# Performance work log

Measured on AMD Instinct MI355X. Metric: run time of the kernel, lower is better.

## Reference

```python
import jax, jax.numpy as jnp
import numpy as np

N, D, E, H, K = 8192, 1024, 8, 256, 2


def setup_inputs() -> dict:
    key = jax.random.key(0)
    ks = jax.random.split(key, 9)
    s = 0.02
    return {
        "x": jax.random.normal(ks[0], (N, D), dtype=jnp.float32),
        "Wg": jax.random.normal(ks[1], (D, E), dtype=jnp.float32) * s,
        "bg": jnp.zeros((E,), dtype=jnp.float32),
        "W1": jax.random.normal(ks[2], (E, D, H), dtype=jnp.float32) * s,
        "b1": jnp.zeros((E, H), dtype=jnp.float32),
        "W2": jax.random.normal(ks[3], (E, H, H), dtype=jnp.float32) * s,
        "b2": jnp.zeros((E, H), dtype=jnp.float32),
        "W3": jax.random.normal(ks[4], (E, H, D), dtype=jnp.float32) * s,
        "b3": jnp.zeros((E, D), dtype=jnp.float32),
    }


def reference(x, Wg, bg, W1, b1, W2, b2, W3, b3):
    # Gating: softmax over experts, then keep only top-k gate values per token.
    gates = jax.nn.softmax(x @ Wg + bg, axis=-1)              # [N, E]
    top_v, top_i = jax.lax.top_k(gates, K)                    # [N, K]
    rows = jnp.arange(gates.shape[0])[:, None]                # [N, 1]
    top_k_gates = jnp.zeros_like(gates).at[rows, top_i].set(top_v)  # [N, E]

    # Dense all-expert MLP (matches original: every expert runs on every token).
    h = jax.nn.relu(jnp.einsum('nd,edh->neh', x, W1) + b1)    # [N, E, H]
    h = jax.nn.relu(jnp.einsum('neh,ehg->neg', h, W2) + b2)   # [N, E, H]  (dropout is eval no-op)
    eo = jax.nn.relu(jnp.einsum('neh,ehd->ned', h, W3) + b3)  # [N, E, D]

    # Combine with masked gates: einsum('...nde,...ne->...nd') with eo in 'ned' layout.
    output = jnp.einsum('ned,ne->nd', eo, top_k_gates)        # [N, D]
    return output
```

## Files before the change

kernel.cpp:

```cpp
#include <hip/hip_runtime.h>
#include <math.h>

#define NTOK 8192
#define DDIM 1024
#define NEXP 8
#define HDIM 256
#define TOPK 2
#define PADM 128
#define CAPS (NTOK * TOPK + NEXP * PADM)
#define NT64  (CAPS / 64)
#define NT128 (CAPS / 128)

typedef __attribute__((ext_vector_type(8))) __bf16 bf16x8;
typedef __attribute__((ext_vector_type(4))) float f32x4;

#define GLDS16(g, s)                                                      \
    __builtin_amdgcn_global_load_lds(                                     \
        (const __attribute__((address_space(1))) void*)(g),               \
        (__attribute__((address_space(3))) void*)(s), 16, 0, 0)

static constexpr size_t OFF_TOFF = 128;
static constexpr size_t OFF_ZBUF = 4096;
static constexpr size_t OFF_T2E  = 8192;
static constexpr size_t OFF_T2G  = OFF_T2E + (size_t)NTOK * TOPK * 4;
static constexpr size_t OFF_SLOT = OFF_T2G + (size_t)NTOK * TOPK * 4;
static constexpr size_t OFF_TOK  = OFF_SLOT + (size_t)NTOK * TOPK * 4;
static constexpr size_t OFF_GAT  = OFF_TOK + (size_t)CAPS * 4;
static constexpr size_t OFF_XB   = (OFF_GAT + (size_t)CAPS * 4 + 255) & ~(size_t)255;
static constexpr size_t OFF_W1T  = OFF_XB  + (size_t)NTOK * DDIM * 2;
static constexpr size_t OFF_W2T  = OFF_W1T + (size_t)NEXP * DDIM * HDIM * 2;
static constexpr size_t OFF_W3T  = OFF_W2T + (size_t)NEXP * HDIM * HDIM * 2;
static constexpr size_t OFF_H2   = OFF_W3T + (size_t)NEXP * HDIM * DDIM * 2;
static constexpr size_t OFF_H3   = OFF_H2  + (size_t)CAPS * HDIM * 2;

static __device__ __forceinline__ unsigned short f2b(float f) {
    __bf16 h = (__bf16)f;
    return __builtin_bit_cast(unsigned short, h);
}
static __device__ __forceinline__ float b2f(unsigned short u) {
    return __builtin_bit_cast(float, ((unsigned)u) << 16);
}

__global__ __launch_bounds__(256) void gate_trans(
    const float* __restrict__ x, const float* __restrict__ Wg,
    const float* __restrict__ bg, unsigned short* __restrict__ xb,
    int* __restrict__ top2e, float* __restrict__ top2g,
    const float* __restrict__ W1, const float* __restrict__ W2,
    const float* __restrict__ W3, __bf16* __restrict__ w1t,
    __bf16* __restrict__ w2t, __bf16* __restrict__ w3t)
{
    __shared__ __align__(16) float sh[NEXP * DDIM];
    const int tid = threadIdx.x;

    if (blockIdx.x < 256) {
        for (int d = tid; d < DDIM; d += 256) {
            const float4 w0 = *(const float4*)(Wg + (size_t)d * NEXP);
            const float4 w1 = *(const float4*)(Wg + (size_t)d * NEXP + 4);
            sh[0 * DDIM + d] = w0.x; sh[1 * DDIM + d] = w0.y;
            sh[2 * DDIM + d] = w0.z; sh[3 * DDIM + d] = w0.w;
            sh[4 * DDIM + d] = w1.x; sh[5 * DDIM + d] = w1.y;
            sh[6 * DDIM + d] = w1.z; sh[7 * DDIM + d] = w1.w;
        }
        __syncthreads();

        const int n = (blockIdx.y * 256 + blockIdx.x) * 4 + (tid >> 6);
        const int lane = tid & 63;
        const float* xr = x + (size_t)n * DDIM;
        unsigned short* xbr = xb + (size_t)n * DDIM;

        float acc[NEXP];
#pragma unroll
        for (int e = 0; e < NEXP; ++e) acc[e] = 0.f;

#pragma unroll
        for (int it = 0; it < 4; ++it) {
            const int d = it * 256 + lane * 4;
            const float4 xv = *(const float4*)(xr + d);
            ushort4 u;
            u.x = f2b(xv.x); u.y = f2b(xv.y); u.z = f2b(xv.z); u.w = f2b(xv.w);
            *(ushort4*)(xbr + d) = u;
#pragma unroll
            for (int e = 0; e < NEXP; ++e) {
                const float4 wt = *(const float4*)(sh + e * DDIM + d);
                acc[e] = fmaf(xv.x, wt.x, acc[e]);
                acc[e] = fmaf(xv.y, wt.y, acc[e]);
                acc[e] = fmaf(xv.z, wt.z, acc[e]);
                acc[e] = fmaf(xv.w, wt.w, acc[e]);
            }
        }
#pragma unroll
        for (int off = 32; off > 0; off >>= 1)
#pragma unroll
            for (int e = 0; e < NEXP; ++e) acc[e] += __shfl_down(acc[e], off, 64);

        if (lane == 0) {
            float v[NEXP], mx = -1e30f;
#pragma unroll
            for (int e = 0; e < NEXP; ++e) { v[e] = acc[e] + bg[e]; mx = fmaxf(mx, v[e]); }
            float p[NEXP], s = 0.f;
#pragma unroll
            for (int e = 0; e < NEXP; ++e) { p[e] = expf(v[e] - mx); s += p[e]; }
            const float inv = 1.f / s;
#pragma unroll
            for (int e = 0; e < NEXP; ++e) p[e] *= inv;
            int i0 = 0;
#pragma unroll
            for (int e = 1; e < NEXP; ++e) if (p[e] > p[i0]) i0 = e;
            int i1 = (i0 == 0) ? 1 : 0;
#pragma unroll
            for (int e = 0; e < NEXP; ++e) if (e != i0 && p[e] > p[i1]) i1 = e;
            top2e[n * 2 + 0] = i0;  top2e[n * 2 + 1] = i1;
            top2g[n * 2 + 0] = p[i0]; top2g[n * 2 + 1] = p[i1];
        }
    } else {
        const int e = blockIdx.y;
        int bt = blockIdx.x - 256;
        const float* Wi; __bf16* Wo; int R, C, xt, yt;
        if (bt < 256)      { Wi = W1; Wo = w1t; R = DDIM; C = HDIM; xt = bt & 7;  yt = bt >> 3; }
        else if (bt < 320) { bt -= 256; Wi = W2; Wo = w2t; R = HDIM; C = HDIM; xt = bt & 7;  yt = bt >> 3; }
        else               { bt -= 320; Wi = W3; Wo = w3t; R = HDIM; C = DDIM; xt = bt & 31; yt = bt >> 5; }
        const int r0 = yt * 32, c0 = xt * 32;
        const int tx = tid & 31, ty = tid >> 5;
        const float* Wie = Wi + (size_t)e * R * C;
        __bf16* Woe = Wo + (size_t)e * C * R;
#pragma unroll
        for (int j = 0; j < 4; ++j)
            sh[(ty + j * 8) * 33 + tx] = Wie[(size_t)(r0 + ty + j * 8) * C + c0 + tx];
        __syncthreads();
#pragma unroll
        for (int j = 0; j < 4; ++j)
            Woe[(size_t)(c0 + ty + j * 8) * R + r0 + tx] = (__bf16)sh[tx * 33 + ty + j * 8];
    }
}

__global__ __launch_bounds__(1024) void route(
    const int* __restrict__ top2e, const float* __restrict__ top2g,
    int* __restrict__ toff, int* __restrict__ tok, float* __restrict__ gat,
    int* __restrict__ slotof, float* __restrict__ zbuf)
{
    const int tid = threadIdx.x;
    const int wv = tid >> 6, ln = tid & 63;
    __shared__ int   waveTot[16][NEXP];
    __shared__ int   waveBase[16][NEXP];
    __shared__ int   totS[NEXP];
    __shared__ int   toffS[NEXP + 1];
    __shared__ short excS[1024][NEXP];

    zbuf[tid] = 0.f;

    int myE[16]; float myG[16];
    const int4*   pe = (const int4*)(top2e + tid * 16);
    const float4* pg = (const float4*)(top2g + tid * 16);
#pragma unroll
    for (int q = 0; q < 4; ++q) {
        const int4 v = pe[q];
        myE[q * 4 + 0] = v.x; myE[q * 4 + 1] = v.y;
        myE[q * 4 + 2] = v.z; myE[q * 4 + 3] = v.w;
        const float4 g = pg[q];
        myG[q * 4 + 0] = g.x; myG[q * 4 + 1] = g.y;
        myG[q * 4 + 2] = g.z; myG[q * 4 + 3] = g.w;
    }

#pragma unroll
    for (int e = 0; e < NEXP; ++e) {
        int c = 0;
#pragma unroll
        for (int j = 0; j < 16; ++j) c += (myE[j] == e);
        int inc = c;
#pragma unroll
        for (int off = 1; off < 64; off <<= 1) {
            const int t = __shfl_up(inc, off, 64);
            if (ln >= off) inc += t;
        }
        excS[tid][e] = (short)(inc - c);
        if (ln == 63) waveTot[wv][e] = inc;
    }
    __syncthreads();

    if (tid < NEXP) {
        int b = 0;
#pragma unroll
        for (int w = 0; w < 16; ++w) {
            const int t = waveTot[w][tid];
            waveBase[w][tid] = b;
            b += t;
        }
        totS[tid] = b;
    }
    __syncthreads();

    if (tid == 0) {
        int acc = 0;
#pragma unroll
        for (int e = 0; e < NEXP; ++e) {
            toffS[e] = acc;
            acc += (totS[e] + PADM - 1) & ~(PADM - 1);
        }
        toffS[NEXP] = acc;
#pragma unroll
        for (int e = 0; e <= NEXP; ++e) toff[e] = toffS[e];
    }
    __syncthreads();

#pragma unroll
    for (int j = 0; j < 16; ++j) {
        int pre = 0;
#pragma unroll
        for (int j2 = 0; j2 < j; ++j2) pre += (myE[j2] == myE[j]);
        const int e = myE[j];
        const int slot = toffS[e] + waveBase[wv][e] + (int)excS[tid][e] + pre;
        const int i = tid * 16 + j;
        tok[slot] = i >> 1;
        gat[slot] = myG[j];
        slotof[i] = slot;
    }

#pragma unroll
    for (int e = 0; e < NEXP; ++e) {
        const int begin = toffS[e] + totS[e];
        const int end   = toffS[e + 1];
        for (int i = begin + tid; i < end; i += 1024) {
            tok[i] = -1;
            gat[i] = 0.f;
        }
    }
}

__global__ __launch_bounds__(256) void egemm12(
    const __bf16* __restrict__ xb, const __bf16* __restrict__ w1t,
    const __bf16* __restrict__ w2t, const float* __restrict__ b1,
    const float* __restrict__ b2, const int* __restrict__ toff,
    const int* __restrict__ tok, const char* __restrict__ zbuf,
    __bf16* __restrict__ h2)
{
    const int total = toff[NEXP];
    const int slot0 = blockIdx.x * 64;
    if (slot0 >= total) return;
    int e = 0;
    while (toff[e + 1] <= slot0) ++e;

    __shared__ __align__(16) char smem[73728];
    char* AsB = smem;
    char* BsB = smem + 8192;
    char* H1s = smem + 40960;

    const int tid  = threadIdx.x;
    const int lane = tid & 63;
    const int wid  = tid >> 6;

    const int srow  = tid >> 3;
    const int sslot = tid & 7;
    const int ks    = sslot ^ (srow & 7);

    const __bf16* We1 = w1t + (size_t)e * HDIM * DDIM;
    const char* ap[2];
#pragma unroll
    for (int i = 0; i < 2; ++i) {
        const int t = tok[slot0 + i * 32 + srow];
        ap[i] = (t >= 0) ? (const char*)(xb + (size_t)t * DDIM + ks * 8) : zbuf;
    }
    const char* bp1[8];
#pragma unroll
    for (int i = 0; i < 8; ++i)
        bp1[i] = (const char*)(We1 + (size_t)(i * 32 + srow) * DDIM + ks * 8);

    const int llo = lane & 15, lhi = lane >> 4;
    const int m7 = llo & 7;
    int abyte[4], bbyte[4];
#pragma unroll
    for (int m = 0; m < 4; ++m) {
        abyte[m] = (m * 16 + llo) * 128;
        bbyte[m] = (wid * 64 + m * 16 + llo) * 128;
    }

    f32x4 acc[4][4];
#pragma unroll
    for (int m = 0; m < 4; ++m)
#pragma unroll
        for (int n = 0; n < 4; ++n) acc[m][n] = (f32x4){0.f, 0.f, 0.f, 0.f};

    for (int k0 = 0; k0 < DDIM; k0 += 64) {
        const size_t kb = (size_t)k0 * 2;
        GLDS16(ap[0] + kb, AsB + tid * 16);
        GLDS16(ap[1] + kb, AsB + 4096 + tid * 16);
#pragma unroll
        for (int i = 0; i < 8; ++i)
            GLDS16(bp1[i] + kb, BsB + i * 4096 + tid * 16);
        __syncthreads();
#pragma unroll
        for (int kk = 0; kk < 2; ++kk) {
            const int sl = ((kk << 2) + lhi) ^ m7;
            bf16x8 af[4], bfr[4];
#pragma unroll
            for (int m = 0; m < 4; ++m) af[m]  = *(const bf16x8*)(AsB + abyte[m] + (sl << 4));
#pragma unroll
            for (int n = 0; n < 4; ++n) bfr[n] = *(const bf16x8*)(BsB + bbyte[n] + (sl << 4));
#pragma unroll
            for (int m = 0; m < 4; ++m)
#pragma unroll
                for (int n = 0; n < 4; ++n)
                    acc[m][n] = __builtin_amdgcn_mfma_f32_16x16x32_bf16(
                        af[m], bfr[n], acc[m][n], 0, 0, 0);
        }
        __syncthreads();
    }

    {
        const float* be1 = b1 + (size_t)e * HDIM;
#pragma unroll
        for (int n = 0; n < 4; ++n) {
            const int col = wid * 64 + n * 16 + llo;
            const float bb = be1[col];
            const int colbyte = (col & 7) * 2;
            const int slice = col >> 3;
#pragma unroll
            for (int m = 0; m < 4; ++m) {
#pragma unroll
                for (int j = 0; j < 4; ++j) {
                    const int r = m * 16 + lhi * 4 + j;
                    const float v = fmaxf(acc[m][n][j] + bb, 0.f);
                    *(__bf16*)(H1s + r * 512 + ((slice ^ (r & 7)) << 4) + colbyte) = (__bf16)v;
                }
                acc[m][n] = (f32x4){0.f, 0.f, 0.f, 0.f};
            }
        }
    }
    __syncthreads();

    const __bf16* We2 = w2t + (size_t)e * HDIM * HDIM;
    const char* bp2[8];
#pragma unroll
    for (int i = 0; i < 8; ++i)
        bp2[i] = (const char*)(We2 + (size_t)(i * 32 + srow) * HDIM + ks * 8);

    for (int k2 = 0; k2 < 4; ++k2) {
        const size_t kb = (size_t)k2 * 128;
#pragma unroll
        for (int i = 0; i < 8; ++i)
            GLDS16(bp2[i] + kb, BsB + i * 4096 + tid * 16);
        __syncthreads();
#pragma unroll
        for (int kk = 0; kk < 2; ++kk) {
            const int slB = ((kk << 2) + lhi) ^ m7;
            const int sA  = k2 * 8 + (kk << 2) + lhi;
            const int slA = sA ^ m7;
            bf16x8 af[4], bfr[4];
#pragma unroll
            for (int m = 0; m < 4; ++m)
                af[m] = *(const bf16x8*)(H1s + (m * 16 + llo) * 512 + (slA << 4));
#pragma unroll
            for (int n = 0; n < 4; ++n)
                bfr[n] = *(const bf16x8*)(BsB + bbyte[n] + (slB << 4));
#pragma unroll
            for (int m = 0; m < 4; ++m)
#pragma unroll
                for (int n = 0; n < 4; ++n)
                    acc[m][n] = __builtin_amdgcn_mfma_f32_16x16x32_bf16(
                        af[m], bfr[n], acc[m][n], 0, 0, 0);
        }
        __syncthreads();
    }

    {
        const float* be2 = b2 + (size_t)e * HDIM;
#pragma unroll
        for (int n = 0; n < 4; ++n) {
            const int col = wid * 64 + n * 16 + llo;
            const float bb = be2[col];
#pragma unroll
            for (int m = 0; m < 4; ++m) {
#pragma unroll
                for (int j = 0; j < 4; ++j) {
                    const int r = slot0 + m * 16 + lhi * 4 + j;
                    h2[(size_t)r * HDIM + col] = (__bf16)fmaxf(acc[m][n][j] + bb, 0.f);
                }
            }
        }
    }
}

template<int KDIM, int NCOL>
__global__ __launch_bounds__(256) void egemm3(
    const __bf16* __restrict__ Ain, const __bf16* __restrict__ Wt,
    const float* __restrict__ ball, const int* __restrict__ toff,
    const float* __restrict__ gat, __bf16* __restrict__ Out)
{
    const int total = toff[NEXP];
    const int slot0 = blockIdx.y * 128;
    if (slot0 >= total) return;
    int e = 0;
    while (toff[e + 1] <= slot0) ++e;
    const int col0 = blockIdx.x * 128;

    __shared__ __align__(16) char smem[32768];
    char* AsB = smem;
    char* BsB = smem + 16384;

    const int tid  = threadIdx.x;
    const int lane = tid & 63;
    const int wid  = tid >> 6;
    const int wr = wid >> 1, wc = wid & 1;

    const int srow  = tid >> 3;
    const int sslot = tid & 7;
    const int ks    = sslot ^ (srow & 7);
    const __bf16* We = Wt + (size_t)e * NCOL * KDIM;
    const char* ap[4];
    const char* bp[4];
#pragma unroll
    for (int i = 0; i < 4; ++i) {
        const int row = i * 32 + srow;
        ap[i] = (const char*)(Ain + (size_t)(slot0 + row) * KDIM + ks * 8);
        bp[i] = (const char*)(We + (size_t)(col0 + row) * KDIM + ks * 8);
    }

    const int llo = lane & 15, lhi = lane >> 4;
    const int m7 = llo & 7;
    int abyte[4], bbyte[4];
#pragma unroll
    for (int m = 0; m < 4; ++m) {
        abyte[m] = (wr * 64 + m * 16 + llo) * 128;
        bbyte[m] = (wc * 64 + m * 16 + llo) * 128;
    }

    f32x4 acc[4][4];
#pragma unroll
    for (int m = 0; m < 4; ++m)
#pragma unroll
        for (int n = 0; n < 4; ++n) acc[m][n] = (f32x4){0.f, 0.f, 0.f, 0.f};

    for (int k0 = 0; k0 < KDIM; k0 += 64) {
        const size_t kb = (size_t)k0 * 2;
#pragma unroll
        for (int i = 0; i < 4; ++i)
            GLDS16(ap[i] + kb, AsB + i * 4096 + wid * 1024);
#pragma unroll
        for (int i = 0; i < 4; ++i)
            GLDS16(bp[i] + kb, BsB + i * 4096 + wid * 1024);
        __syncthreads();
#pragma unroll
        for (int kk = 0; kk < 2; ++kk) {
            const int sl = ((kk << 2) + lhi) ^ m7;
            bf16x8 af[4], bfr[4];
#pragma unroll
            for (int m = 0; m < 4; ++m) af[m]  = *(const bf16x8*)(AsB + abyte[m] + (sl << 4));
#pragma unroll
            for (int n = 0; n < 4; ++n) bfr[n] = *(const bf16x8*)(BsB + bbyte[n] + (sl << 4));
#pragma unroll
            for (int m = 0; m < 4; ++m)
#pragma unroll
                for (int n = 0; n < 4; ++n)
                    acc[m][n] = __builtin_amdgcn_mfma_f32_16x16x32_bf16(
                        af[m], bfr[n], acc[m][n], 0, 0, 0);
        }
        __syncthreads();
    }

    const float* be = ball + (size_t)e * NCOL;
#pragma unroll
    for (int m = 0; m < 4; ++m) {
        const int rbase = slot0 + wr * 64 + m * 16 + lhi * 4;
        float g[4];
#pragma unroll
        for (int j = 0; j < 4; ++j) g[j] = gat[rbase + j];
#pragma unroll
        for (int n = 0; n < 4; ++n) {
            const int col = col0 + wc * 64 + n * 16 + llo;
            const float bb = be[col];
#pragma unroll
            for (int j = 0; j < 4; ++j) {
                const float v = fmaxf(acc[m][n][j] + bb, 0.f) * g[j];
                Out[(size_t)(rbase + j) * NCOL + col] = (__bf16)v;
            }
        }
    }
}

__global__ __launch_bounds__(256) void combine(
    const unsigned short* __restrict__ h3, const int* __restrict__ slotof,
    float* __restrict__ out)
{
    const int n = blockIdx.x;
    const int c = threadIdx.x * 4;
    const int s0 = slotof[n * 2], s1 = slotof[n * 2 + 1];
    const ushort4 a = *(const ushort4*)(h3 + (size_t)s0 * DDIM + c);
    const ushort4 b = *(const ushort4*)(h3 + (size_t)s1 * DDIM + c);
    float4 o;
    o.x = b2f(a.x) + b2f(b.x);
    o.y = b2f(a.y) + b2f(b.y);
    o.z = b2f(a.z) + b2f(b.z);
    o.w = b2f(a.w) + b2f(b.w);
    *(float4*)(out + (size_t)n * DDIM + c) = o;
}

extern "C" void kernel_launch(void* const* d_in, const int* in_sizes, int n_in,
                              void* d_out, int out_size, void* d_ws, size_t ws_size,
                              hipStream_t stream)
{
    const float* x  = (const float*)d_in[0];
    const float* Wg = (const float*)d_in[1];
    const float* bg = (const float*)d_in[2];
    const float* W1 = (const float*)d_in[3];
    const float* b1 = (const float*)d_in[4];
    const float* W2 = (const float*)d_in[5];
    const float* b2 = (const float*)d_in[6];
    const float* W3 = (const float*)d_in[7];
    const float* b3 = (const float*)d_in[8];
    float* out = (float*)d_out;

    char* ws = (char*)d_ws;
    int*   toff   = (int*)(ws + OFF_TOFF);
    char*  zbuf   = ws + OFF_ZBUF;
    int*   top2e  = (int*)(ws + OFF_T2E);
    float* top2g  = (float*)(ws + OFF_T2G);
    int*   slotof = (int*)(ws + OFF_SLOT);
    int*   tok    = (int*)(ws + OFF_TOK);
    float* gat    = (float*)(ws + OFF_GAT);
    unsigned short* xbu = (unsigned short*)(ws + OFF_XB);
    __bf16* xb  = (__bf16*)(ws + OFF_XB);
    __bf16* w1t = (__bf16*)(ws + OFF_W1T);
    __bf16* w2t = (__bf16*)(ws + OFF_W2T);
    __bf16* w3t = (__bf16*)(ws + OFF_W3T);
    __bf16* h2  = (__bf16*)(ws + OFF_H2);
    __bf16* h3  = (__bf16*)(ws + OFF_H3);

    gate_trans<<<dim3(832, NEXP), 256, 0, stream>>>(
        x, Wg, bg, xbu, top2e, top2g, W1, W2, W3, w1t, w2t, w3t);
    route<<<1, 1024, 0, stream>>>(top2e, top2g, toff, tok, gat, slotof, (float*)zbuf);

    egemm12<<<NT64, 256, 0, stream>>>(xb, w1t, w2t, b1, b2, toff, tok, zbuf, h2);
    egemm3<HDIM, DDIM><<<dim3(DDIM / 128, NT128), 256, 0, stream>>>(
        h2, w3t, b3, toff, gat, h3);

    combine<<<NTOK, 256, 0, stream>>>((const unsigned short*)h3, slotof, out);
}
```

Before: 106.8 us.

## Fuse top-k combine into expert GEMM3 epilogue via atomic adds

Removes the separate combine kernel and the bf16 h3 intermediate buffer. The third expert GEMM now scatters its gated output straight into the fp32 output with unsafeAtomicAdd, indexed by token, and skips padded slots. The output is zeroed inside the gate/transpose kernel. This saves one launch plus a write and re-read of the h3 buffer and the slot map, at the cost of scattered fp32 atomics (two per output element) and an extra full zeroing pass over the output.

```diff
diff --git a/kernel.cpp b/kernel.cpp
--- a/kernel.cpp
+++ b/kernel.cpp
@@ -23,22 +23,17 @@
 static constexpr size_t OFF_ZBUF = 4096;
 static constexpr size_t OFF_T2E  = 8192;
 static constexpr size_t OFF_T2G  = OFF_T2E + (size_t)NTOK * TOPK * 4;
-static constexpr size_t OFF_SLOT = OFF_T2G + (size_t)NTOK * TOPK * 4;
-static constexpr size_t OFF_TOK  = OFF_SLOT + (size_t)NTOK * TOPK * 4;
+static constexpr size_t OFF_TOK  = OFF_T2G + (size_t)NTOK * TOPK * 4;
 static constexpr size_t OFF_GAT  = OFF_TOK + (size_t)CAPS * 4;
 static constexpr size_t OFF_XB   = (OFF_GAT + (size_t)CAPS * 4 + 255) & ~(size_t)255;
 static constexpr size_t OFF_W1T  = OFF_XB  + (size_t)NTOK * DDIM * 2;
 static constexpr size_t OFF_W2T  = OFF_W1T + (size_t)NEXP * DDIM * HDIM * 2;
 static constexpr size_t OFF_W3T  = OFF_W2T + (size_t)NEXP * HDIM * HDIM * 2;
 static constexpr size_t OFF_H2   = OFF_W3T + (size_t)NEXP * HDIM * DDIM * 2;
-static constexpr size_t OFF_H3   = OFF_H2  + (size_t)CAPS * HDIM * 2;
 
 static __device__ __forceinline__ unsigned short f2b(float f) {
     __bf16 h = (__bf16)f;
     return __builtin_bit_cast(unsigned short, h);
-}
-static __device__ __forceinline__ float b2f(unsigned short u) {
-    return __builtin_bit_cast(float, ((unsigned)u) << 16);
 }
 
 __global__ __launch_bounds__(256) void gate_trans(
@@ -47,10 +42,18 @@
     int* __restrict__ top2e, float* __restrict__ top2g,
     const float* __restrict__ W1, const float* __restrict__ W2,
     const float* __restrict__ W3, __bf16* __restrict__ w1t,
-    __bf16* __restrict__ w2t, __bf16* __restrict__ w3t)
+    __bf16* __restrict__ w2t, __bf16* __restrict__ w3t,
+    float* __restrict__ outz)
 {
     __shared__ __align__(16) float sh[NEXP * DDIM];
     const int tid = threadIdx.x;
+
+    {
+        float4* o4 = (float4*)outz;
+        const int gid = (blockIdx.y * 832 + blockIdx.x) * 256 + tid;
+        for (size_t i = gid; i < (size_t)NTOK * DDIM / 4; i += 6656 * 256)
+            o4[i] = make_float4(0.f, 0.f, 0.f, 0.f);
+    }
 
     if (blockIdx.x < 256) {
         for (int d = tid; d < DDIM; d += 256) {
@@ -136,7 +139,7 @@
 __global__ __launch_bounds__(1024) void route(
     const int* __restrict__ top2e, const float* __restrict__ top2g,
     int* __restrict__ toff, int* __restrict__ tok, float* __restrict__ gat,
-    int* __restrict__ slotof, float* __restrict__ zbuf)
+    float* __restrict__ zbuf)
 {
     const int tid = threadIdx.x;
     const int wv = tid >> 6, ln = tid & 63;
@@ -212,7 +215,6 @@
         const int i = tid * 16 + j;
         tok[slot] = i >> 1;
         gat[slot] = myG[j];
-        slotof[i] = slot;
     }
 
 #pragma unroll
@@ -257,7 +259,8 @@
 #pragma unroll
     for (int i = 0; i < 2; ++i) {
         const int t = tok[slot0 + i * 32 + srow];
-        ap[i] = (t >= 0) ? (const char*)(xb + (size_t)t * DDIM + ks * 8) : zbuf;
+        ap[i] = (t >= 0) ? (const char*)(xb + (size_t)t * DDIM + ks * 8)
+                         : (const char*)zbuf;
     }
     const char* bp1[8];
 #pragma unroll
@@ -383,7 +386,8 @@
 __global__ __launch_bounds__(256) void egemm3(
     const __bf16* __restrict__ Ain, const __bf16* __restrict__ Wt,
     const float* __restrict__ ball, const int* __restrict__ toff,
-    const float* __restrict__ gat, __bf16* __restrict__ Out)
+    const int* __restrict__ tok, const float* __restrict__ gat,
+    float* __restrict__ out)
 {
     const int total = toff[NEXP];
     const int slot0 = blockIdx.y * 128;
@@ -460,37 +464,21 @@
 #pragma unroll
     for (int m = 0; m < 4; ++m) {
         const int rbase = slot0 + wr * 64 + m * 16 + lhi * 4;
-        float g[4];
-#pragma unroll
-        for (int j = 0; j < 4; ++j) g[j] = gat[rbase + j];
+        float g[4]; int t[4];
+#pragma unroll
+        for (int j = 0; j < 4; ++j) { g[j] = gat[rbase + j]; t[j] = tok[rbase + j]; }
 #pragma unroll
         for (int n = 0; n < 4; ++n) {
             const int col = col0 + wc * 64 + n * 16 + llo;
             const float bb = be[col];
 #pragma unroll
             for (int j = 0; j < 4; ++j) {
+                if (t[j] < 0) continue;
                 const float v = fmaxf(acc[m][n][j] + bb, 0.f) * g[j];
-                Out[(size_t)(rbase + j) * NCOL + col] = (__bf16)v;
+                unsafeAtomicAdd(out + (size_t)t[j] * NCOL + col, v);
             }
         }
     }
-}
-
-__global__ __launch_bounds__(256) void combine(
-    const unsigned short* __restrict__ h3, const int* __restrict__ slotof,
-    float* __restrict__ out)
-{
-    const int n = blockIdx.x;
-    const int c = threadIdx.x * 4;
-    const int s0 = slotof[n * 2], s1 = slotof[n * 2 + 1];
-    const ushort4 a = *(const ushort4*)(h3 + (size_t)s0 * DDIM + c);
-    const ushort4 b = *(const ushort4*)(h3 + (size_t)s1 * DDIM + c);
-    float4 o;
-    o.x = b2f(a.x) + b2f(b.x);
-    o.y = b2f(a.y) + b2f(b.y);
-    o.z = b2f(a.z) + b2f(b.z);
-    o.w = b2f(a.w) + b2f(b.w);
-    *(float4*)(out + (size_t)n * DDIM + c) = o;
 }
 
 extern "C" void kernel_launch(void* const* d_in, const int* in_sizes, int n_in,
@@ -513,7 +501,6 @@
     char*  zbuf   = ws + OFF_ZBUF;
     int*   top2e  = (int*)(ws + OFF_T2E);
     float* top2g  = (float*)(ws + OFF_T2G);
-    int*   slotof = (int*)(ws + OFF_SLOT);
     int*   tok    = (int*)(ws + OFF_TOK);
     float* gat    = (float*)(ws + OFF_GAT);
     unsigned short* xbu = (unsigned short*)(ws + OFF_XB);
@@ -522,15 +509,12 @@
     __bf16* w2t = (__bf16*)(ws + OFF_W2T);
     __bf16* w3t = (__bf16*)(ws + OFF_W3T);
     __bf16* h2  = (__bf16*)(ws + OFF_H2);
-    __bf16* h3  = (__bf16*)(ws + OFF_H3);
 
     gate_trans<<<dim3(832, NEXP), 256, 0, stream>>>(
-        x, Wg, bg, xbu, top2e, top2g, W1, W2, W3, w1t, w2t, w3t);
-    route<<<1, 1024, 0, stream>>>(top2e, top2g, toff, tok, gat, slotof, (float*)zbuf);
+        x, Wg, bg, xbu, top2e, top2g, W1, W2, W3, w1t, w2t, w3t, out);
+    route<<<1, 1024, 0, stream>>>(top2e, top2g, toff, tok, gat, (float*)zbuf);
 
     egemm12<<<NT64, 256, 0, stream>>>(xb, w1t, w2t, b1, b2, toff, tok, zbuf, h2);
     egemm3<HDIM, DDIM><<<dim3(DDIM / 128, NT128), 256, 0, stream>>>(
-        h2, w3t, b3, toff, gat, h3);
-
-    combine<<<NTOK, 256, 0, stream>>>((const unsigned short*)h3, slotof, out);
+        h2, w3t, b3, toff, tok, gat, out);
 }
```

New measurement: 144.7 us. +35.4%, slower.
